# Kernel optimization log

Measured on AMD Instinct MI355X. Metric: run time of the kernel, lower is better.

The kernel has to match this reference:

```python
import jax, jax.numpy as jnp
import numpy as np

L = 6          # number of GNN layers
D = 128        # feature_dim (d_model)
H = 4          # num_heads (hardcoded in AttentionalPropagation)
DH = D // H    # per-head dim
N = 2048       # number of segments/keypoints per frame
B = 1          # batch
NAMES = ["self", "cross"] * (L // 2)
EPS = 1e-5     # InstanceNorm1d eps


def _conv1(W, b, x):
    # Conv1d kernel_size=1: W [out,in], x [b,in,n] -> [b,out,n]
    return jnp.einsum('oi,bin->bon', W, x) + b[None, :, None]


def _inorm(x):
    # InstanceNorm1d (affine=False): normalize over the length axis per (batch, channel)
    m = jnp.mean(x, axis=-1, keepdims=True)
    v = jnp.mean((x - m) ** 2, axis=-1, keepdims=True)
    return (x - m) * jax.lax.rsqrt(v + EPS)


def _attn_block(x, src, p):
    Wq, bq, Wk, bk, Wv, bv, Wm, bm, W1, b1, W2, b2 = p
    b_dim, _, n = x.shape
    # view(b, dim, heads, -1): channel axis split as (DH, H)
    q = _conv1(Wq, bq, x).reshape(b_dim, DH, H, -1)
    k = _conv1(Wk, bk, src).reshape(b_dim, DH, H, -1)
    v = _conv1(Wv, bv, src).reshape(b_dim, DH, H, -1)
    scores = jnp.einsum('bdhn,bdhm->bhnm', q, k) / jnp.sqrt(jnp.asarray(DH, x.dtype))
    prob = jax.nn.softmax(scores, axis=-1)
    msg = jnp.einsum('bhnm,bdhm->bdhn', prob, v).reshape(b_dim, D, -1)
    msg = _conv1(Wm, bm, msg)
    # MLP([2D, 2D, D]): Conv1d -> InstanceNorm1d -> ReLU -> Conv1d
    h = _conv1(W1, b1, jnp.concatenate([x, msg], axis=1))
    h = jax.nn.relu(_inorm(h))
    return _conv1(W2, b2, h)


def setup_inputs() -> dict:
    key = jax.random.key(0)
    ks = jax.random.split(key, 14)
    s = 0.05
    f32 = jnp.float32
    return {
        "desc0": jax.random.normal(ks[0], (B, D, N), f32),
        "desc1": jax.random.normal(ks[1], (B, D, N), f32),
        "Wq": jax.random.normal(ks[2], (L, D, D), f32) * s,
        "bq": jnp.zeros((L, D), f32),
        "Wk": jax.random.normal(ks[3], (L, D, D), f32) * s,
        "bk": jnp.zeros((L, D), f32),
        "Wv": jax.random.normal(ks[4], (L, D, D), f32) * s,
        "bv": jnp.zeros((L, D), f32),
        "Wm": jax.random.normal(ks[5], (L, D, D), f32) * s,
        "bm": jnp.zeros((L, D), f32),
        "W1": jax.random.normal(ks[6], (L, 2 * D, 2 * D), f32) * s,
        "b1": jnp.zeros((L, 2 * D), f32),
        "W2": jax.random.normal(ks[7], (L, D, 2 * D), f32) * s,
        "b2": jnp.zeros((L, D), f32),  # nn.init.constant_(mlp[-1].bias, 0.0)
    }


def reference(desc0, desc1, Wq, bq, Wk, bk, Wv, bv, Wm, bm, W1, b1, W2, b2):
    params = (Wq, bq, Wk, bk, Wv, bv, Wm, bm, W1, b1, W2, b2)
    for l in range(L):
        p = tuple(a[l] for a in params)
        if NAMES[l] == 'cross':
            src0, src1 = desc1, desc0
        else:
            src0, src1 = desc0, desc1
        delta0 = _attn_block(desc0, src0, p)
        delta1 = _attn_block(desc1, src1, p)
        desc0 = desc0 + delta0
        desc1 = desc1 + delta1
    return desc0, desc1
```

## Files before the change

### kernel.cpp

```cpp
#include <hip/hip_runtime.h>

#define NN 2048
#define DDIM 128
#define NHEAD 4
#define DH 32
#define NL 6

typedef __attribute__((ext_vector_type(8))) __bf16 bf16x8;
typedef __attribute__((ext_vector_type(4))) float f32x4;

__device__ __forceinline__ unsigned int f2bf(float x) {
  unsigned int u = __float_as_uint(x);
  u += 0x7fff + ((u >> 16) & 1);
  return u >> 16;
}
__device__ __forceinline__ unsigned int pk2(float a, float b) {
  return f2bf(a) | (f2bf(b) << 16);
}
__device__ __forceinline__ float bf2f(unsigned short u) {
  return __uint_as_float(((unsigned int)u) << 16);
}

__global__ __launch_bounds__(256) void setup_kernel(
    const float* __restrict__ Wq, const float* __restrict__ Wk,
    const float* __restrict__ Wv, const float* __restrict__ Wm,
    const float* __restrict__ W1, const float* __restrict__ W2,
    const float* __restrict__ bmv, const float* __restrict__ b1,
    const float* __restrict__ desc0, const float* __restrict__ desc1,
    unsigned short* __restrict__ Wqkv, unsigned short* __restrict__ Wb2,
    unsigned short* __restrict__ Wmix, float* __restrict__ b1m,
    unsigned short* __restrict__ dT0, unsigned short* __restrict__ dT1,
    float* __restrict__ o0, float* __restrict__ o1) {
  __shared__ __align__(16) unsigned char ARENA[17408];
  const int bid = blockIdx.x;
  const int t = threadIdx.x;

  if (bid < 672) {
    int idx = (bid * 256 + t) * 4;
    if (idx >= 688128) return;
    const float* src; unsigned short* dst; int soff, doff;
    if (idx < 98304)       { src = Wq; soff = idx; dst = Wqkv; doff = idx; }
    else if (idx < 196608) { src = Wk; soff = idx - 98304; dst = Wqkv; doff = idx; }
    else if (idx < 294912) { src = Wv; soff = idx - 196608; dst = Wqkv; doff = idx; }
    else if (idx < 491520) { src = W2; soff = idx - 294912; dst = Wb2; doff = soff; }
    else {
      int f = idx - 491520;
      int l = f >> 15, rem = f & 32767;
      int i = rem >> 7, c = rem & 127;
      src = W1; soff = (l << 16) + (i << 8) + c;
      dst = Wmix; doff = (l << 16) + (i << 8) + c;
    }
    float4 v = *(const float4*)&src[soff];
    uint2 p = { pk2(v.x, v.y), pk2(v.z, v.w) };
    *(uint2*)&dst[doff] = p;
  } else if (bid < 720) {
    const int b = bid - 672;
    const int jb = b & 1, ib = (b >> 1) & 3, l = b >> 3;
    const int bj = jb * 64, bi = ib * 64;
    float* Ws = (float*)ARENA;
    float* Xs = (float*)ARENA + 2080;
    const int ti = (t >> 4) << 2;
    const int tj = (t & 15) << 2;
    float acc[4][4] = {{0.f}};
    for (int k0 = 0; k0 < 128; k0 += 32) {
#pragma unroll
      for (int i = 0; i < 8; ++i) {
        int e = t + i * 256;
        int ii = e >> 5, kk = e & 31;
        Ws[kk * 65 + ii] = W1[(size_t)(l << 16) + (bi + ii) * 256 + 128 + k0 + kk];
      }
#pragma unroll
      for (int i = 0; i < 2; ++i) {
        int e = t + i * 256;
        int r = e >> 4, c4 = e & 15;
        *(float4*)&Xs[r * 64 + c4 * 4] =
            *(const float4*)&Wm[(size_t)l * 16384 + (k0 + r) * 128 + bj + c4 * 4];
      }
      __syncthreads();
#pragma unroll
      for (int kk = 0; kk < 32; ++kk) {
        float a[4];
        a[0] = Ws[kk * 65 + ti]; a[1] = Ws[kk * 65 + ti + 1];
        a[2] = Ws[kk * 65 + ti + 2]; a[3] = Ws[kk * 65 + ti + 3];
        float4 b4 = *(const float4*)&Xs[kk * 64 + tj];
        float bb[4] = {b4.x, b4.y, b4.z, b4.w};
#pragma unroll
        for (int i = 0; i < 4; ++i)
#pragma unroll
          for (int j = 0; j < 4; ++j) acc[i][j] += a[i] * bb[j];
      }
      __syncthreads();
    }
#pragma unroll
    for (int i = 0; i < 4; ++i) {
      uint2 p = { pk2(acc[i][0], acc[i][1]), pk2(acc[i][2], acc[i][3]) };
      *(uint2*)&Wmix[(size_t)(l << 16) + (bi + ti + i) * 256 + 128 + bj + tj] = p;
    }
    if (jb == 0 && ib == 0) {
      float a = b1[l * 256 + t];
      const float* wr = &W1[(size_t)(l << 16) + t * 256 + 128];
      const float* bp = &bmv[l * 128];
      for (int k = 0; k < 128; k += 4)
        a += wr[k] * bp[k] + wr[k + 1] * bp[k + 1] + wr[k + 2] * bp[k + 2] + wr[k + 3] * bp[k + 3];
      b1m[l * 256 + t] = a;
    }
  } else {
    const int b = bid - 720;
    const float* D = (b >> 5) ? desc1 : desc0;
    unsigned short* T = (b >> 5) ? dT1 : dT0;
    float* O = (b >> 5) ? o1 : o0;
    const int n0 = (b & 31) * 64;
    unsigned short* L = (unsigned short*)ARENA;
#pragma unroll
    for (int i = 0; i < 8; ++i) {
      int idx = t + i * 256;
      int c = idx >> 4, nj = (idx & 15) * 4;
      float4 v = *(const float4*)&D[(size_t)c * NN + n0 + nj];
      *(float4*)&O[(size_t)c * NN + n0 + nj] = v;
      L[(nj + 0) * 136 + c] = (unsigned short)f2bf(v.x);
      L[(nj + 1) * 136 + c] = (unsigned short)f2bf(v.y);
      L[(nj + 2) * 136 + c] = (unsigned short)f2bf(v.z);
      L[(nj + 3) * 136 + c] = (unsigned short)f2bf(v.w);
    }
    __syncthreads();
#pragma unroll
    for (int i = 0; i < 4; ++i) {
      int idx = t + i * 256;
      int n = idx >> 4, cj = (idx & 15) * 8;
      uint4 v = *(const uint4*)&L[n * 136 + cj];
      *(uint4*)&T[(size_t)(n0 + n) * 128 + cj] = v;
    }
  }
}

struct MOp {
  const unsigned short* A;
  const float* bias;
  const unsigned short* B1;
  const unsigned short* B2;
  unsigned short* Cb;
  float* Cf;
  const float* Sp;
  int ldb, ldc, mode;
};
struct MOps8 { MOp op[8]; };

template <int K>
__global__ __launch_bounds__(256) void gemm_direct_kernel(MOps8 P) {
  const MOp g = P.op[blockIdx.z];
  const int t = threadIdx.x;
  const int w = t >> 6, lane = t & 63;
  const int col = lane & 15, Qd = lane >> 4;
  const int bm = blockIdx.y * 64;
  const int bn = blockIdx.x * 64;

  __shared__ float meanL[256], rstdL[256];
  __shared__ float swS[4][64], swQ[4][64];

  if (g.mode == 4) {
    float s = g.Sp[t * 2], ss = g.Sp[t * 2 + 1];
    float mean = s * (1.0f / NN);
    float var = fmaxf(ss * (1.0f / NN) - mean * mean, 0.f);
    meanL[t] = mean;
    rstdL[t] = rsqrtf(var + 1e-5f);
  }
  if (g.mode == 0 && g.Cf && blockIdx.x == 0 && blockIdx.y == 0) {
    g.Cf[t] = 0.f;
    g.Cf[t + 256] = 0.f;
  }
  __syncthreads();

  const int n = bn + w * 16 + col;
  f32x4 acc[4];
#pragma unroll
  for (int mt = 0; mt < 4; ++mt) acc[mt] = (f32x4){0.f, 0.f, 0.f, 0.f};

#pragma unroll
  for (int k0 = 0; k0 < K; k0 += 32) {
    bf16x8 af[4];
#pragma unroll
    for (int mt = 0; mt < 4; ++mt)
      af[mt] = *(const bf16x8*)&g.A[(size_t)(bm + mt * 16 + col) * K + k0 + Qd * 8];
    const unsigned short* Bp = g.B1;
    int kk = k0;
    if (g.B2 && k0 >= 128) { Bp = g.B2; kk = k0 - 128; }
    uint4 v = *(const uint4*)&Bp[(size_t)n * g.ldb + kk + Qd * 8];
    if (g.mode == 4) {
      float4 mA = *(const float4*)&meanL[k0 + Qd * 8];
      float4 mB = *(const float4*)&meanL[k0 + Qd * 8 + 4];
      float4 rA = *(const float4*)&rstdL[k0 + Qd * 8];
      float4 rB = *(const float4*)&rstdL[k0 + Qd * 8 + 4];
      union { uint4 q; unsigned short us[8]; } u;
      u.q = v;
      float x0 = fmaxf((bf2f(u.us[0]) - mA.x) * rA.x, 0.f);
      float x1 = fmaxf((bf2f(u.us[1]) - mA.y) * rA.y, 0.f);
      float x2 = fmaxf((bf2f(u.us[2]) - mA.z) * rA.z, 0.f);
      float x3 = fmaxf((bf2f(u.us[3]) - mA.w) * rA.w, 0.f);
      float x4 = fmaxf((bf2f(u.us[4]) - mB.x) * rB.x, 0.f);
      float x5 = fmaxf((bf2f(u.us[5]) - mB.y) * rB.y, 0.f);
      float x6 = fmaxf((bf2f(u.us[6]) - mB.z) * rB.z, 0.f);
      float x7 = fmaxf((bf2f(u.us[7]) - mB.w) * rB.w, 0.f);
      u.q.x = pk2(x0, x1); u.q.y = pk2(x2, x3);
      u.q.z = pk2(x4, x5); u.q.w = pk2(x6, x7);
      v = u.q;
    }
    union { uint4 q; bf16x8 b; } bc;
    bc.q = v;
#pragma unroll
    for (int mt = 0; mt < 4; ++mt)
      acc[mt] = __builtin_amdgcn_mfma_f32_16x16x32_bf16(af[mt], bc.b, acc[mt], 0, 0, 0);
  }

#pragma unroll
  for (int mt = 0; mt < 4; ++mt) {
    const int c0 = bm + mt * 16 + Qd * 4;
    const float b0 = g.bias[c0], b1 = g.bias[c0 + 1];
    const float b2 = g.bias[c0 + 2], b3 = g.bias[c0 + 3];
    f32x4 a = acc[mt];
    float v0 = a[0] + b0, v1 = a[1] + b1, v2 = a[2] + b2, v3 = a[3] + b3;
    if (g.mode <= 2) {
      if (g.mode == 0) {
        const float sc = 0.25503488f;
        v0 *= sc; v1 *= sc; v2 *= sc; v3 *= sc;
      }
      const int d = c0 >> 2;
      if (g.mode == 1) {
        g.Cb[((size_t)0 * NN + n) * 32 + d] = (unsigned short)f2bf(v0);
        g.Cb[((size_t)1 * NN + n) * 32 + d] = (unsigned short)f2bf(v1);
        g.Cb[((size_t)2 * NN + n) * 32 + d] = (unsigned short)f2bf(v2);
        g.Cb[((size_t)3 * NN + n) * 32 + d] = (unsigned short)f2bf(v3);
      } else {
        g.Cb[(size_t)(0 * 32 + d) * NN + n] = (unsigned short)f2bf(v0);
        g.Cb[(size_t)(1 * 32 + d) * NN + n] = (unsigned short)f2bf(v1);
        g.Cb[(size_t)(2 * 32 + d) * NN + n] = (unsigned short)f2bf(v2);
        g.Cb[(size_t)(3 * 32 + d) * NN + n] = (unsigned short)f2bf(v3);
      }
    } else if (g.mode == 5) {
      uint2 pv = { pk2(v0, v1), pk2(v2, v3) };
      *(uint2*)&g.Cb[(size_t)n * g.ldc + c0] = pv;
      float sA[4] = {v0, v1, v2, v3};
      float sQ[4] = {v0 * v0, v1 * v1, v2 * v2, v3 * v3};
#pragma unroll
      for (int r = 0; r < 4; ++r) {
#pragma unroll
        for (int off = 1; off < 16; off <<= 1) {
          sA[r] += __shfl_xor(sA[r], off);
          sQ[r] += __shfl_xor(sQ[r], off);
        }
      }
      if (col == 0) {
#pragma unroll
        for (int r = 0; r < 4; ++r) {
          swS[w][mt * 16 + Qd * 4 + r] = sA[r];
          swQ[w][mt * 16 + Qd * 4 + r] = sQ[r];
        }
      }
    } else {
      float* dp = g.Cf;
      float o0 = dp[(size_t)(c0 + 0) * NN + n] + v0;
      float o1 = dp[(size_t)(c0 + 1) * NN + n] + v1;
      float o2 = dp[(size_t)(c0 + 2) * NN + n] + v2;
      float o3 = dp[(size_t)(c0 + 3) * NN + n] + v3;
      dp[(size_t)(c0 + 0) * NN + n] = o0;
      dp[(size_t)(c0 + 1) * NN + n] = o1;
      dp[(size_t)(c0 + 2) * NN + n] = o2;
      dp[(size_t)(c0 + 3) * NN + n] = o3;
      uint2 pv = { pk2(o0, o1), pk2(o2, o3) };
      *(uint2*)&g.Cb[(size_t)n * g.ldc + c0] = pv;
    }
  }
  if (g.mode == 5) {
    __syncthreads();
    if (t < 64) {
      float a = swS[0][t] + swS[1][t] + swS[2][t] + swS[3][t];
      float b = swQ[0][t] + swQ[1][t] + swQ[2][t] + swQ[3][t];
      atomicAdd(&g.Cf[(bm + t) * 2], a);
      atomicAdd(&g.Cf[(bm + t) * 2 + 1], b);
    }
  }
}

__global__ __launch_bounds__(256, 4) void attn_mfma_kernel(
    const unsigned short* __restrict__ Qb0, const unsigned short* __restrict__ Kt0,
    const unsigned short* __restrict__ Vb0, const unsigned short* __restrict__ Qb1,
    const unsigned short* __restrict__ Kt1, const unsigned short* __restrict__ Vb1,
    unsigned short* __restrict__ mgT0, unsigned short* __restrict__ mgT1, int cross) {
  const int z = blockIdx.y, desc = z >> 2, h = z & 3;
  const int t = threadIdx.x;
  const int wid = t >> 6, lane = t & 63;
  const int col = lane & 15, Qd = lane >> 4;
  const int qb = blockIdx.x * 16;

  const unsigned short* Qb = desc ? Qb1 : Qb0;
  const int s = cross ? (1 - desc) : desc;
  const unsigned short* Kt = s ? Kt1 : Kt0;
  const unsigned short* Vb = s ? Vb1 : Vb0;

  __shared__ __align__(16) unsigned short SM[7424];
  unsigned short* PW = SM + wid * 640;
  float* fS = (float*)(SM + 2560);

  bf16x8 bq;
  {
    union { unsigned short u[8]; bf16x8 v; } tmp;
#pragma unroll
    for (int j = 0; j < 8; ++j)
      tmp.u[j] = Qb[(size_t)(h * 32 + Qd * 8 + j) * NN + qb + col];
    bq = tmp.v;
  }

  f32x4 o0 = {0.f, 0.f, 0.f, 0.f}, o1 = {0.f, 0.f, 0.f, 0.f};
  float m = -1e30f, l = 0.f;

  const int kq = wid * 512;
#pragma unroll 2
  for (int it = 0; it < 16; ++it) {
    const int k0 = kq + it * 32;
    bf16x8 aK0 = *(const bf16x8*)&Kt[((size_t)h * NN + k0 + col) * 32 + Qd * 8];
    bf16x8 aK1 = *(const bf16x8*)&Kt[((size_t)h * NN + k0 + 16 + col) * 32 + Qd * 8];
    bf16x8 av0 = *(const bf16x8*)&Vb[(size_t)(h * 32 + col) * NN + k0 + Qd * 8];
    bf16x8 av1 = *(const bf16x8*)&Vb[(size_t)(h * 32 + 16 + col) * NN + k0 + Qd * 8];
    f32x4 z4 = {0.f, 0.f, 0.f, 0.f};
    f32x4 s0 = __builtin_amdgcn_mfma_f32_16x16x32_bf16(aK0, bq, z4, 0, 0, 0);
    f32x4 s1 = __builtin_amdgcn_mfma_f32_16x16x32_bf16(aK1, bq, z4, 0, 0, 0);
    float cm = fmaxf(fmaxf(fmaxf(s0[0], s0[1]), fmaxf(s0[2], s0[3])),
                     fmaxf(fmaxf(s1[0], s1[1]), fmaxf(s1[2], s1[3])));
    cm = fmaxf(cm, __shfl_xor(cm, 16));
    cm = fmaxf(cm, __shfl_xor(cm, 32));
    const float mn = fmaxf(m, cm);
    const float alpha = exp2f(m - mn);
    m = mn;
    float p00 = exp2f(s0[0] - mn), p01 = exp2f(s0[1] - mn);
    float p02 = exp2f(s0[2] - mn), p03 = exp2f(s0[3] - mn);
    float p10 = exp2f(s1[0] - mn), p11 = exp2f(s1[1] - mn);
    float p12 = exp2f(s1[2] - mn), p13 = exp2f(s1[3] - mn);
    float us = (p00 + p01) + (p02 + p03) + (p10 + p11) + (p12 + p13);
    us += __shfl_xor(us, 16);
    us += __shfl_xor(us, 32);
    l = l * alpha + us;
    uint2 w0 = { pk2(p00, p01), pk2(p02, p03) };
    uint2 w1 = { pk2(p10, p11), pk2(p12, p13) };
    *(uint2*)&PW[col * 40 + Qd * 4] = w0;
    *(uint2*)&PW[col * 40 + 16 + Qd * 4] = w1;
    bf16x8 pb = *(const bf16x8*)&PW[col * 40 + Qd * 8];
    o0 = o0 * alpha;
    o1 = o1 * alpha;
    o0 = __builtin_amdgcn_mfma_f32_16x16x32_bf16(av0, pb, o0, 0, 0, 0);
    o1 = __builtin_amdgcn_mfma_f32_16x16x32_bf16(av1, pb, o1, 0, 0, 0);
  }

  __syncthreads();
  *(float4*)&fS[wid * 576 + col * 36 + Qd * 4] =
      make_float4(o0[0], o0[1], o0[2], o0[3]);
  *(float4*)&fS[wid * 576 + col * 36 + 16 + Qd * 4] =
      make_float4(o1[0], o1[1], o1[2], o1[3]);
  if (Qd == 0) {
    fS[2304 + wid * 16 + col] = m;
    fS[2368 + wid * 16 + col] = l;
  }
  __syncthreads();
  {
    const int q16 = t >> 4, dg = t & 15;
    float m0 = fS[2304 + q16], m1 = fS[2304 + 16 + q16];
    float m2 = fS[2304 + 32 + q16], m3 = fS[2304 + 48 + q16];
    float M = fmaxf(fmaxf(m0, m1), fmaxf(m2, m3));
    float w0 = exp2f(m0 - M), w1 = exp2f(m1 - M);
    float w2 = exp2f(m2 - M), w3 = exp2f(m3 - M);
    float L = w0 * fS[2368 + q16] + w1 * fS[2368 + 16 + q16] +
              w2 * fS[2368 + 32 + q16] + w3 * fS[2368 + 48 + q16];
    float inv = 1.0f / L;
    unsigned short* T = desc ? mgT1 : mgT0;
    const int q = qb + q16;
#pragma unroll
    for (int r = 0; r < 2; ++r) {
      int d = dg * 2 + r;
      float v = (w0 * fS[0 * 576 + q16 * 36 + d] + w1 * fS[1 * 576 + q16 * 36 + d] +
                 w2 * fS[2 * 576 + q16 * 36 + d] + w3 * fS[3 * 576 + q16 * 36 + d]) * inv;
      T[(size_t)q * 128 + d * 4 + h] = (unsigned short)f2bf(v);
    }
  }
}

extern "C" void kernel_launch(void* const* d_in, const int* in_sizes, int n_in,
                              void* d_out, int out_size, void* d_ws, size_t ws_size,
                              hipStream_t stream) {
  const float* desc0 = (const float*)d_in[0];
  const float* desc1 = (const float*)d_in[1];
  const float* Wq = (const float*)d_in[2];
  const float* bq = (const float*)d_in[3];
  const float* Wk = (const float*)d_in[4];
  const float* bk = (const float*)d_in[5];
  const float* Wv = (const float*)d_in[6];
  const float* bv = (const float*)d_in[7];
  const float* Wm = (const float*)d_in[8];
  const float* bmv = (const float*)d_in[9];
  const float* W1 = (const float*)d_in[10];
  const float* b1 = (const float*)d_in[11];
  const float* W2 = (const float*)d_in[12];
  const float* b2 = (const float*)d_in[13];

  float* out0 = (float*)d_out;
  float* out1 = out0 + (size_t)DDIM * NN;

  float* fws = (float*)d_ws;
  float* Sg0 = fws;
  float* Sg1 = Sg0 + 512;
  float* b1m = Sg1 + 512;
  unsigned short* uws = (unsigned short*)(b1m + 1536);
  unsigned short* dT0 = uws;
  unsigned short* dT1 = uws + 1 * 262144;
  unsigned short* Qb0 = uws + 2 * 262144;
  unsigned short* Qb1 = uws + 3 * 262144;
  unsigned short* Kt0 = uws + 4 * 262144;
  unsigned short* Kt1 = uws + 5 * 262144;
  unsigned short* Vb0 = uws + 6 * 262144;
  unsigned short* Vb1 = uws + 7 * 262144;
  unsigned short* mgT0 = uws + 8 * 262144;
  unsigned short* mgT1 = uws + 9 * 262144;
  unsigned short* HT0 = uws + 10 * 262144;
  unsigned short* HT1 = HT0 + 524288;
  unsigned short* Wqkv = HT1 + 524288;
  unsigned short* Wb2 = Wqkv + 294912;
  unsigned short* Wmix = Wb2 + 196608;

  setup_kernel<<<784, 256, 0, stream>>>(Wq, Wk, Wv, Wm, W1, W2, bmv, b1,
                                        desc0, desc1, Wqkv, Wb2, Wmix, b1m,
                                        dT0, dT1, out0, out1);

  for (int l = 0; l < NL; ++l) {
    const int cross = l & 1;
    const unsigned short* wq = Wqkv + l * 16384;
    const unsigned short* wk = Wqkv + 98304 + l * 16384;
    const unsigned short* wv = Wqkv + 196608 + l * 16384;
    const unsigned short* wmx = Wmix + l * 65536;
    const unsigned short* w2 = Wb2 + l * 32768;
    const float* bqp = bq + (size_t)l * 128;
    const float* bkp = bk + (size_t)l * 128;
    const float* bvp = bv + (size_t)l * 128;
    const float* b1p = b1m + (size_t)l * 256;
    const float* b2p = b2 + (size_t)l * 128;

    MOps8 Pq = {};
    Pq.op[0] = {wq, bqp, dT0, nullptr, Qb0, Sg0, nullptr, 128, 0, 0};
    Pq.op[1] = {wq, bqp, dT1, nullptr, Qb1, Sg1, nullptr, 128, 0, 0};
    Pq.op[2] = {wk, bkp, dT0, nullptr, Kt0, nullptr, nullptr, 128, 0, 1};
    Pq.op[3] = {wk, bkp, dT1, nullptr, Kt1, nullptr, nullptr, 128, 0, 1};
    Pq.op[4] = {wv, bvp, dT0, nullptr, Vb0, nullptr, nullptr, 128, 0, 2};
    Pq.op[5] = {wv, bvp, dT1, nullptr, Vb1, nullptr, nullptr, 128, 0, 2};
    gemm_direct_kernel<128><<<dim3(32, 2, 6), 256, 0, stream>>>(Pq);

    attn_mfma_kernel<<<dim3(128, 8), 256, 0, stream>>>(
        Qb0, Kt0, Vb0, Qb1, Kt1, Vb1, mgT0, mgT1, cross);

    MOps8 P1 = {};
    P1.op[0] = {wmx, b1p, dT0, mgT0, HT0, Sg0, nullptr, 128, 256, 5};
    P1.op[1] = {wmx, b1p, dT1, mgT1, HT1, Sg1, nullptr, 128, 256, 5};
    gemm_direct_kernel<256><<<dim3(32, 4, 2), 256, 0, stream>>>(P1);

    MOps8 P2 = {};
    P2.op[0] = {w2, b2p, HT0, nullptr, dT0, out0, Sg0, 256, 128, 4};
    P2.op[1] = {w2, b2p, HT1, nullptr, dT1, out1, Sg1, 256, 128, 4};
    gemm_direct_kernel<256><<<dim3(32, 2, 2), 256, 0, stream>>>(P2);
  }
}
```

Before: 425.0 us.

## Use two-pass softmax in attention kernel with 64-key tiles

Replaces the online-softmax loop with two passes. The first pass computes QK^T scores only to find the row max. The second pass recomputes the scores, exponentiates against the fixed max and accumulates P·V without per-iteration alpha rescaling or cross-lane shuffles. The key tile grows from 32 to 64 per iteration, and LDS staging for P grows to match. This removes the serial max/sum shuffle reductions and accumulator rescaling from the inner loop, at the cost of loading K twice and computing the score MFMAs twice.

```diff
diff --git a/kernel.cpp b/kernel.cpp
--- a/kernel.cpp
+++ b/kernel.cpp
@@ -296,9 +296,9 @@
   const unsigned short* Kt = s ? Kt1 : Kt0;
   const unsigned short* Vb = s ? Vb1 : Vb0;
 
-  __shared__ __align__(16) unsigned short SM[7424];
-  unsigned short* PW = SM + wid * 640;
-  float* fS = (float*)(SM + 2560);
+  __shared__ __align__(16) unsigned short SM[9472];
+  unsigned short* PW = SM + wid * 1152;
+  float* fS = (float*)(SM + 4608);
 
   bf16x8 bq;
   {
@@ -309,45 +309,76 @@
     bq = tmp.v;
   }
 
-  f32x4 o0 = {0.f, 0.f, 0.f, 0.f}, o1 = {0.f, 0.f, 0.f, 0.f};
-  float m = -1e30f, l = 0.f;
-
   const int kq = wid * 512;
+  const size_t kbase = (size_t)h * NN;
+
+  float m = -1e30f;
 #pragma unroll 2
-  for (int it = 0; it < 16; ++it) {
-    const int k0 = kq + it * 32;
-    bf16x8 aK0 = *(const bf16x8*)&Kt[((size_t)h * NN + k0 + col) * 32 + Qd * 8];
-    bf16x8 aK1 = *(const bf16x8*)&Kt[((size_t)h * NN + k0 + 16 + col) * 32 + Qd * 8];
-    bf16x8 av0 = *(const bf16x8*)&Vb[(size_t)(h * 32 + col) * NN + k0 + Qd * 8];
-    bf16x8 av1 = *(const bf16x8*)&Vb[(size_t)(h * 32 + 16 + col) * NN + k0 + Qd * 8];
+  for (int it = 0; it < 8; ++it) {
+    const int k0 = kq + it * 64;
+    bf16x8 aK0 = *(const bf16x8*)&Kt[(kbase + k0 + col) * 32 + Qd * 8];
+    bf16x8 aK1 = *(const bf16x8*)&Kt[(kbase + k0 + 16 + col) * 32 + Qd * 8];
+    bf16x8 aK2 = *(const bf16x8*)&Kt[(kbase + k0 + 32 + col) * 32 + Qd * 8];
+    bf16x8 aK3 = *(const bf16x8*)&Kt[(kbase + k0 + 48 + col) * 32 + Qd * 8];
     f32x4 z4 = {0.f, 0.f, 0.f, 0.f};
     f32x4 s0 = __builtin_amdgcn_mfma_f32_16x16x32_bf16(aK0, bq, z4, 0, 0, 0);
     f32x4 s1 = __builtin_amdgcn_mfma_f32_16x16x32_bf16(aK1, bq, z4, 0, 0, 0);
-    float cm = fmaxf(fmaxf(fmaxf(s0[0], s0[1]), fmaxf(s0[2], s0[3])),
-                     fmaxf(fmaxf(s1[0], s1[1]), fmaxf(s1[2], s1[3])));
-    cm = fmaxf(cm, __shfl_xor(cm, 16));
-    cm = fmaxf(cm, __shfl_xor(cm, 32));
-    const float mn = fmaxf(m, cm);
-    const float alpha = exp2f(m - mn);
-    m = mn;
-    float p00 = exp2f(s0[0] - mn), p01 = exp2f(s0[1] - mn);
-    float p02 = exp2f(s0[2] - mn), p03 = exp2f(s0[3] - mn);
-    float p10 = exp2f(s1[0] - mn), p11 = exp2f(s1[1] - mn);
-    float p12 = exp2f(s1[2] - mn), p13 = exp2f(s1[3] - mn);
-    float us = (p00 + p01) + (p02 + p03) + (p10 + p11) + (p12 + p13);
-    us += __shfl_xor(us, 16);
-    us += __shfl_xor(us, 32);
-    l = l * alpha + us;
+    f32x4 s2 = __builtin_amdgcn_mfma_f32_16x16x32_bf16(aK2, bq, z4, 0, 0, 0);
+    f32x4 s3 = __builtin_amdgcn_mfma_f32_16x16x32_bf16(aK3, bq, z4, 0, 0, 0);
+    float c01 = fmaxf(fmaxf(fmaxf(s0[0], s0[1]), fmaxf(s0[2], s0[3])),
+                      fmaxf(fmaxf(s1[0], s1[1]), fmaxf(s1[2], s1[3])));
+    float c23 = fmaxf(fmaxf(fmaxf(s2[0], s2[1]), fmaxf(s2[2], s2[3])),
+                      fmaxf(fmaxf(s3[0], s3[1]), fmaxf(s3[2], s3[3])));
+    m = fmaxf(m, fmaxf(c01, c23));
+  }
+  m = fmaxf(m, __shfl_xor(m, 16));
+  m = fmaxf(m, __shfl_xor(m, 32));
+
+  f32x4 o0 = {0.f, 0.f, 0.f, 0.f}, o1 = {0.f, 0.f, 0.f, 0.f};
+  float l = 0.f;
+#pragma unroll 2
+  for (int it = 0; it < 8; ++it) {
+    const int k0 = kq + it * 64;
+    bf16x8 aK0 = *(const bf16x8*)&Kt[(kbase + k0 + col) * 32 + Qd * 8];
+    bf16x8 aK1 = *(const bf16x8*)&Kt[(kbase + k0 + 16 + col) * 32 + Qd * 8];
+    bf16x8 aK2 = *(const bf16x8*)&Kt[(kbase + k0 + 32 + col) * 32 + Qd * 8];
+    bf16x8 aK3 = *(const bf16x8*)&Kt[(kbase + k0 + 48 + col) * 32 + Qd * 8];
+    bf16x8 av00 = *(const bf16x8*)&Vb[(size_t)(h * 32 + col) * NN + k0 + Qd * 8];
+    bf16x8 av01 = *(const bf16x8*)&Vb[(size_t)(h * 32 + col) * NN + k0 + 32 + Qd * 8];
+    bf16x8 av10 = *(const bf16x8*)&Vb[(size_t)(h * 32 + 16 + col) * NN + k0 + Qd * 8];
+    bf16x8 av11 = *(const bf16x8*)&Vb[(size_t)(h * 32 + 16 + col) * NN + k0 + 32 + Qd * 8];
+    f32x4 z4 = {0.f, 0.f, 0.f, 0.f};
+    f32x4 s0 = __builtin_amdgcn_mfma_f32_16x16x32_bf16(aK0, bq, z4, 0, 0, 0);
+    f32x4 s1 = __builtin_amdgcn_mfma_f32_16x16x32_bf16(aK1, bq, z4, 0, 0, 0);
+    f32x4 s2 = __builtin_amdgcn_mfma_f32_16x16x32_bf16(aK2, bq, z4, 0, 0, 0);
+    f32x4 s3 = __builtin_amdgcn_mfma_f32_16x16x32_bf16(aK3, bq, z4, 0, 0, 0);
+    float p00 = exp2f(s0[0] - m), p01 = exp2f(s0[1] - m);
+    float p02 = exp2f(s0[2] - m), p03 = exp2f(s0[3] - m);
+    float p10 = exp2f(s1[0] - m), p11 = exp2f(s1[1] - m);
+    float p12 = exp2f(s1[2] - m), p13 = exp2f(s1[3] - m);
+    float p20 = exp2f(s2[0] - m), p21 = exp2f(s2[1] - m);
+    float p22 = exp2f(s2[2] - m), p23 = exp2f(s2[3] - m);
+    float p30 = exp2f(s3[0] - m), p31 = exp2f(s3[1] - m);
+    float p32 = exp2f(s3[2] - m), p33 = exp2f(s3[3] - m);
+    l += ((p00 + p01) + (p02 + p03)) + ((p10 + p11) + (p12 + p13)) +
+         ((p20 + p21) + (p22 + p23)) + ((p30 + p31) + (p32 + p33));
     uint2 w0 = { pk2(p00, p01), pk2(p02, p03) };
     uint2 w1 = { pk2(p10, p11), pk2(p12, p13) };
-    *(uint2*)&PW[col * 40 + Qd * 4] = w0;
-    *(uint2*)&PW[col * 40 + 16 + Qd * 4] = w1;
-    bf16x8 pb = *(const bf16x8*)&PW[col * 40 + Qd * 8];
-    o0 = o0 * alpha;
-    o1 = o1 * alpha;
-    o0 = __builtin_amdgcn_mfma_f32_16x16x32_bf16(av0, pb, o0, 0, 0, 0);
-    o1 = __builtin_amdgcn_mfma_f32_16x16x32_bf16(av1, pb, o1, 0, 0, 0);
-  }
+    uint2 w2 = { pk2(p20, p21), pk2(p22, p23) };
+    uint2 w3 = { pk2(p30, p31), pk2(p32, p33) };
+    *(uint2*)&PW[col * 72 + Qd * 4] = w0;
+    *(uint2*)&PW[col * 72 + 16 + Qd * 4] = w1;
+    *(uint2*)&PW[col * 72 + 32 + Qd * 4] = w2;
+    *(uint2*)&PW[col * 72 + 48 + Qd * 4] = w3;
+    bf16x8 pb0 = *(const bf16x8*)&PW[col * 72 + Qd * 8];
+    bf16x8 pb1 = *(const bf16x8*)&PW[col * 72 + 32 + Qd * 8];
+    o0 = __builtin_amdgcn_mfma_f32_16x16x32_bf16(av00, pb0, o0, 0, 0, 0);
+    o0 = __builtin_amdgcn_mfma_f32_16x16x32_bf16(av01, pb1, o0, 0, 0, 0);
+    o1 = __builtin_amdgcn_mfma_f32_16x16x32_bf16(av10, pb0, o1, 0, 0, 0);
+    o1 = __builtin_amdgcn_mfma_f32_16x16x32_bf16(av11, pb1, o1, 0, 0, 0);
+  }
+  l += __shfl_xor(l, 16);
+  l += __shfl_xor(l, 32);
 
   __syncthreads();
   *(float4*)&fS[wid * 576 + col * 36 + Qd * 4] =
```

Result: slower. 461.1 us (+8.5%).

## Fuse W2 projection with next layer's QKV projection into one tail kernel

Applied to the files above, without the earlier changes.

Adds a fused kernel that applies instance-norm and ReLU to the hidden activations, runs the W2 GEMM with the residual update, stages the new bf16 descriptors in shared memory, and computes the next layer's Q/K/V projections in the same block. This removes one kernel launch per layer and the global round trip of the updated descriptors. The per-layer statistics buffers are now pre-zeroed once in setup instead of inside the QKV GEMM. The trade-off is 16-column tiles, so each block re-reads the full weight matrices, and the Q/K/V stores are scattered.

```diff
diff --git a/kernel.cpp b/kernel.cpp
--- a/kernel.cpp
+++ b/kernel.cpp
@@ -30,7 +30,8 @@
     unsigned short* __restrict__ Wqkv, unsigned short* __restrict__ Wb2,
     unsigned short* __restrict__ Wmix, float* __restrict__ b1m,
     unsigned short* __restrict__ dT0, unsigned short* __restrict__ dT1,
-    float* __restrict__ o0, float* __restrict__ o1) {
+    float* __restrict__ o0, float* __restrict__ o1,
+    float* __restrict__ SgAll) {
   __shared__ __align__(16) unsigned char ARENA[17408];
   const int bid = blockIdx.x;
   const int t = threadIdx.x;
@@ -104,7 +105,7 @@
         a += wr[k] * bp[k] + wr[k + 1] * bp[k + 1] + wr[k + 2] * bp[k + 2] + wr[k + 3] * bp[k + 3];
       b1m[l * 256 + t] = a;
     }
-  } else {
+  } else if (bid < 784) {
     const int b = bid - 720;
     const float* D = (b >> 5) ? desc1 : desc0;
     unsigned short* T = (b >> 5) ? dT1 : dT0;
@@ -130,6 +131,9 @@
       uint4 v = *(const uint4*)&L[n * 136 + cj];
       *(uint4*)&T[(size_t)(n0 + n) * 128 + cj] = v;
     }
+  } else {
+    float4 z = make_float4(0.f, 0.f, 0.f, 0.f);
+    *(float4*)&SgAll[(bid - 784) * 1024 + t * 4] = z;
   }
 }
 
@@ -163,10 +167,6 @@
     float var = fmaxf(ss * (1.0f / NN) - mean * mean, 0.f);
     meanL[t] = mean;
     rstdL[t] = rsqrtf(var + 1e-5f);
-  }
-  if (g.mode == 0 && g.Cf && blockIdx.x == 0 && blockIdx.y == 0) {
-    g.Cf[t] = 0.f;
-    g.Cf[t + 256] = 0.f;
   }
   __syncthreads();
 
@@ -276,6 +276,136 @@
       float b = swQ[0][t] + swQ[1][t] + swQ[2][t] + swQ[3][t];
       atomicAdd(&g.Cf[(bm + t) * 2], a);
       atomicAdd(&g.Cf[(bm + t) * 2 + 1], b);
+    }
+  }
+}
+
+struct FDesc {
+  const unsigned short* HT; const float* Sp; float* outF; unsigned short* dT;
+  unsigned short* Qb; unsigned short* Kt; unsigned short* Vb;
+};
+struct FArgs {
+  FDesc d[2];
+  const unsigned short *W2l, *Wql, *Wkl, *Wvl;
+  const float *b2l, *bql, *bkl, *bvl;
+};
+
+__global__ __launch_bounds__(256) void fused_tail_kernel(FArgs F) {
+  const FDesc g = F.d[blockIdx.y];
+  const int t = threadIdx.x;
+  const int w = t >> 6, lane = t & 63;
+  const int col = lane & 15, Qd = lane >> 4;
+  const int nb = blockIdx.x * 16;
+  const int n = nb + col;
+
+  __shared__ float meanL[256], rstdL[256];
+  __shared__ __align__(16) unsigned short dTs[16 * 136];
+
+  {
+    float s = g.Sp[t * 2], ss = g.Sp[t * 2 + 1];
+    float mean = s * (1.0f / NN);
+    float var = fmaxf(ss * (1.0f / NN) - mean * mean, 0.f);
+    meanL[t] = mean;
+    rstdL[t] = rsqrtf(var + 1e-5f);
+  }
+  __syncthreads();
+
+  f32x4 accA[2];
+  accA[0] = (f32x4){0.f, 0.f, 0.f, 0.f};
+  accA[1] = (f32x4){0.f, 0.f, 0.f, 0.f};
+#pragma unroll
+  for (int k0 = 0; k0 < 256; k0 += 32) {
+    uint4 v = *(const uint4*)&g.HT[(size_t)n * 256 + k0 + Qd * 8];
+    float4 mA = *(const float4*)&meanL[k0 + Qd * 8];
+    float4 mB = *(const float4*)&meanL[k0 + Qd * 8 + 4];
+    float4 rA = *(const float4*)&rstdL[k0 + Qd * 8];
+    float4 rB = *(const float4*)&rstdL[k0 + Qd * 8 + 4];
+    union { uint4 q; unsigned short us[8]; } u;
+    u.q = v;
+    float x0 = fmaxf((bf2f(u.us[0]) - mA.x) * rA.x, 0.f);
+    float x1 = fmaxf((bf2f(u.us[1]) - mA.y) * rA.y, 0.f);
+    float x2 = fmaxf((bf2f(u.us[2]) - mA.z) * rA.z, 0.f);
+    float x3 = fmaxf((bf2f(u.us[3]) - mA.w) * rA.w, 0.f);
+    float x4 = fmaxf((bf2f(u.us[4]) - mB.x) * rB.x, 0.f);
+    float x5 = fmaxf((bf2f(u.us[5]) - mB.y) * rB.y, 0.f);
+    float x6 = fmaxf((bf2f(u.us[6]) - mB.z) * rB.z, 0.f);
+    float x7 = fmaxf((bf2f(u.us[7]) - mB.w) * rB.w, 0.f);
+    u.q.x = pk2(x0, x1); u.q.y = pk2(x2, x3);
+    u.q.z = pk2(x4, x5); u.q.w = pk2(x6, x7);
+    union { uint4 q; bf16x8 b; } bc;
+    bc.q = u.q;
+#pragma unroll
+    for (int mt = 0; mt < 2; ++mt) {
+      bf16x8 af = *(const bf16x8*)&F.W2l[(size_t)(w * 32 + mt * 16 + col) * 256 + k0 + Qd * 8];
+      accA[mt] = __builtin_amdgcn_mfma_f32_16x16x32_bf16(af, bc.b, accA[mt], 0, 0, 0);
+    }
+  }
+#pragma unroll
+  for (int mt = 0; mt < 2; ++mt) {
+    const int c0 = w * 32 + mt * 16 + Qd * 4;
+    f32x4 a = accA[mt];
+    float o0 = g.outF[(size_t)(c0 + 0) * NN + n] + a[0] + F.b2l[c0 + 0];
+    float o1 = g.outF[(size_t)(c0 + 1) * NN + n] + a[1] + F.b2l[c0 + 1];
+    float o2 = g.outF[(size_t)(c0 + 2) * NN + n] + a[2] + F.b2l[c0 + 2];
+    float o3 = g.outF[(size_t)(c0 + 3) * NN + n] + a[3] + F.b2l[c0 + 3];
+    g.outF[(size_t)(c0 + 0) * NN + n] = o0;
+    g.outF[(size_t)(c0 + 1) * NN + n] = o1;
+    g.outF[(size_t)(c0 + 2) * NN + n] = o2;
+    g.outF[(size_t)(c0 + 3) * NN + n] = o3;
+    unsigned short s0 = (unsigned short)f2bf(o0), s1 = (unsigned short)f2bf(o1);
+    unsigned short s2 = (unsigned short)f2bf(o2), s3 = (unsigned short)f2bf(o3);
+    dTs[col * 136 + c0 + 0] = s0;
+    dTs[col * 136 + c0 + 1] = s1;
+    dTs[col * 136 + c0 + 2] = s2;
+    dTs[col * 136 + c0 + 3] = s3;
+    uint2 pv = { ((unsigned int)s0) | (((unsigned int)s1) << 16),
+                 ((unsigned int)s2) | (((unsigned int)s3) << 16) };
+    *(uint2*)&g.dT[(size_t)n * 128 + c0] = pv;
+  }
+  __syncthreads();
+
+  f32x4 accB[6];
+#pragma unroll
+  for (int f = 0; f < 6; ++f) accB[f] = (f32x4){0.f, 0.f, 0.f, 0.f};
+#pragma unroll
+  for (int k0 = 0; k0 < 128; k0 += 32) {
+    bf16x8 bq = *(const bf16x8*)&dTs[col * 136 + k0 + Qd * 8];
+#pragma unroll
+    for (int f = 0; f < 6; ++f) {
+      const int idx = w * 6 + f;
+      const int op = idx >> 3, mt = idx & 7;
+      const unsigned short* W = (op == 0) ? F.Wql : (op == 1) ? F.Wkl : F.Wvl;
+      bf16x8 af = *(const bf16x8*)&W[(size_t)(mt * 16 + col) * 128 + k0 + Qd * 8];
+      accB[f] = __builtin_amdgcn_mfma_f32_16x16x32_bf16(af, bq, accB[f], 0, 0, 0);
+    }
+  }
+#pragma unroll
+  for (int f = 0; f < 6; ++f) {
+    const int idx = w * 6 + f;
+    const int op = idx >> 3, mt = idx & 7;
+    const float* bias = (op == 0) ? F.bql : (op == 1) ? F.bkl : F.bvl;
+    const int c0 = mt * 16 + Qd * 4;
+    f32x4 a = accB[f];
+    float v0 = a[0] + bias[c0], v1 = a[1] + bias[c0 + 1];
+    float v2 = a[2] + bias[c0 + 2], v3 = a[3] + bias[c0 + 3];
+    const int d = c0 >> 2;
+    if (op == 0) {
+      const float sc = 0.25503488f;
+      v0 *= sc; v1 *= sc; v2 *= sc; v3 *= sc;
+      g.Qb[(size_t)(0 * 32 + d) * NN + n] = (unsigned short)f2bf(v0);
+      g.Qb[(size_t)(1 * 32 + d) * NN + n] = (unsigned short)f2bf(v1);
+      g.Qb[(size_t)(2 * 32 + d) * NN + n] = (unsigned short)f2bf(v2);
+      g.Qb[(size_t)(3 * 32 + d) * NN + n] = (unsigned short)f2bf(v3);
+    } else if (op == 1) {
+      g.Kt[((size_t)0 * NN + n) * 32 + d] = (unsigned short)f2bf(v0);
+      g.Kt[((size_t)1 * NN + n) * 32 + d] = (unsigned short)f2bf(v1);
+      g.Kt[((size_t)2 * NN + n) * 32 + d] = (unsigned short)f2bf(v2);
+      g.Kt[((size_t)3 * NN + n) * 32 + d] = (unsigned short)f2bf(v3);
+    } else {
+      g.Vb[(size_t)(0 * 32 + d) * NN + n] = (unsigned short)f2bf(v0);
+      g.Vb[(size_t)(1 * 32 + d) * NN + n] = (unsigned short)f2bf(v1);
+      g.Vb[(size_t)(2 * 32 + d) * NN + n] = (unsigned short)f2bf(v2);
+      g.Vb[(size_t)(3 * 32 + d) * NN + n] = (unsigned short)f2bf(v3);
     }
   }
 }
@@ -403,9 +533,8 @@
   float* out1 = out0 + (size_t)DDIM * NN;
 
   float* fws = (float*)d_ws;
-  float* Sg0 = fws;
-  float* Sg1 = Sg0 + 512;
-  float* b1m = Sg1 + 512;
+  float* SgAll = fws;
+  float* b1m = SgAll + 6144;
   unsigned short* uws = (unsigned short*)(b1m + 1536);
   unsigned short* dT0 = uws;
   unsigned short* dT1 = uws + 1 * 262144;
@@ -423,31 +552,29 @@
   unsigned short* Wb2 = Wqkv + 294912;
   unsigned short* Wmix = Wb2 + 196608;
 
-  setup_kernel<<<784, 256, 0, stream>>>(Wq, Wk, Wv, Wm, W1, W2, bmv, b1,
+  setup_kernel<<<790, 256, 0, stream>>>(Wq, Wk, Wv, Wm, W1, W2, bmv, b1,
                                         desc0, desc1, Wqkv, Wb2, Wmix, b1m,
-                                        dT0, dT1, out0, out1);
+                                        dT0, dT1, out0, out1, SgAll);
+
+  {
+    MOps8 Pq = {};
+    Pq.op[0] = {Wqkv, bq, dT0, nullptr, Qb0, nullptr, nullptr, 128, 0, 0};
+    Pq.op[1] = {Wqkv, bq, dT1, nullptr, Qb1, nullptr, nullptr, 128, 0, 0};
+    Pq.op[2] = {Wqkv + 98304, bk, dT0, nullptr, Kt0, nullptr, nullptr, 128, 0, 1};
+    Pq.op[3] = {Wqkv + 98304, bk, dT1, nullptr, Kt1, nullptr, nullptr, 128, 0, 1};
+    Pq.op[4] = {Wqkv + 196608, bv, dT0, nullptr, Vb0, nullptr, nullptr, 128, 0, 2};
+    Pq.op[5] = {Wqkv + 196608, bv, dT1, nullptr, Vb1, nullptr, nullptr, 128, 0, 2};
+    gemm_direct_kernel<128><<<dim3(32, 2, 6), 256, 0, stream>>>(Pq);
+  }
 
   for (int l = 0; l < NL; ++l) {
     const int cross = l & 1;
-    const unsigned short* wq = Wqkv + l * 16384;
-    const unsigned short* wk = Wqkv + 98304 + l * 16384;
-    const unsigned short* wv = Wqkv + 196608 + l * 16384;
     const unsigned short* wmx = Wmix + l * 65536;
     const unsigned short* w2 = Wb2 + l * 32768;
-    const float* bqp = bq + (size_t)l * 128;
-    const float* bkp = bk + (size_t)l * 128;
-    const float* bvp = bv + (size_t)l * 128;
     const float* b1p = b1m + (size_t)l * 256;
     const float* b2p = b2 + (size_t)l * 128;
-
-    MOps8 Pq = {};
-    Pq.op[0] = {wq, bqp, dT0, nullptr, Qb0, Sg0, nullptr, 128, 0, 0};
-    Pq.op[1] = {wq, bqp, dT1, nullptr, Qb1, Sg1, nullptr, 128, 0, 0};
-    Pq.op[2] = {wk, bkp, dT0, nullptr, Kt0, nullptr, nullptr, 128, 0, 1};
-    Pq.op[3] = {wk, bkp, dT1, nullptr, Kt1, nullptr, nullptr, 128, 0, 1};
-    Pq.op[4] = {wv, bvp, dT0, nullptr, Vb0, nullptr, nullptr, 128, 0, 2};
-    Pq.op[5] = {wv, bvp, dT1, nullptr, Vb1, nullptr, nullptr, 128, 0, 2};
-    gemm_direct_kernel<128><<<dim3(32, 2, 6), 256, 0, stream>>>(Pq);
+    float* Sg0 = SgAll + l * 1024;
+    float* Sg1 = Sg0 + 512;
 
     attn_mfma_kernel<<<dim3(128, 8), 256, 0, stream>>>(
         Qb0, Kt0, Vb0, Qb1, Kt1, Vb1, mgT0, mgT1, cross);
@@ -457,9 +584,24 @@
     P1.op[1] = {wmx, b1p, dT1, mgT1, HT1, Sg1, nullptr, 128, 256, 5};
     gemm_direct_kernel<256><<<dim3(32, 4, 2), 256, 0, stream>>>(P1);
 
-    MOps8 P2 = {};
-    P2.op[0] = {w2, b2p, HT0, nullptr, dT0, out0, Sg0, 256, 128, 4};
-    P2.op[1] = {w2, b2p, HT1, nullptr, dT1, out1, Sg1, 256, 128, 4};
-    gemm_direct_kernel<256><<<dim3(32, 2, 2), 256, 0, stream>>>(P2);
-  }
-}
+    if (l < NL - 1) {
+      FArgs F;
+      F.d[0] = {HT0, Sg0, out0, dT0, Qb0, Kt0, Vb0};
+      F.d[1] = {HT1, Sg1, out1, dT1, Qb1, Kt1, Vb1};
+      F.W2l = w2;
+      F.Wql = Wqkv + (l + 1) * 16384;
+      F.Wkl = Wqkv + 98304 + (l + 1) * 16384;
+      F.Wvl = Wqkv + 196608 + (l + 1) * 16384;
+      F.b2l = b2p;
+      F.bql = bq + (size_t)(l + 1) * 128;
+      F.bkl = bk + (size_t)(l + 1) * 128;
+      F.bvl = bv + (size_t)(l + 1) * 128;
+      fused_tail_kernel<<<dim3(128, 2), 256, 0, stream>>>(F);
+    } else {
+      MOps8 P2 = {};
+      P2.op[0] = {w2, b2p, HT0, nullptr, dT0, out0, Sg0, 256, 128, 4};
+      P2.op[1] = {w2, b2p, HT1, nullptr, dT1, out1, Sg1, 256, 128, 4};
+      gemm_direct_kernel<256><<<dim3(32, 2, 2), 256, 0, stream>>>(P2);
+    }
+  }
+}
```

Measured after the change: 402.7 us. 1.06x faster.
